# Kernel tuning notes

Measured on AMD Instinct MI355X. Metric: run time of the kernel, lower is better.

Reference implementation:

```python
import jax, jax.numpy as jnp
import numpy as np

D, NH, DH, DHR, DC = 2048, 16, 128, 64, 1024
B, L = 2, 2048
EPS = 1e-6


def _rms(x, w):
    return x * jax.lax.rsqrt(jnp.mean(x * x, axis=-1, keepdims=True) + EPS) * w


def _rope_tables(seq_len, dim, dtype):
    inv_freq = 1.0 / (10000.0 ** (jnp.arange(0, dim, 2, dtype=jnp.float32) / dim))
    freqs = jnp.arange(seq_len, dtype=jnp.float32)[:, None] * inv_freq[None, :]  # [L, dim/2]
    emb = jnp.concatenate([freqs, freqs], axis=-1)                               # [L, dim]
    return jnp.cos(emb).astype(dtype), jnp.sin(emb).astype(dtype)


def _apply_rope(x, cos, sin):
    # x: [B, H, L, dhr]
    half = x.shape[-1] // 2
    x1, x2 = x[..., :half], x[..., half:]
    rot = jnp.concatenate([-x2, x1], axis=-1)
    return x * cos[None, None] + rot * sin[None, None]


def setup_inputs() -> dict:
    key = jax.random.key(0)
    ks = jax.random.split(key, 14)
    s = 0.02
    inp = {
        "x": jax.random.normal(ks[0], (B, L, D), dtype=jnp.float32),
        "W_DKV": jax.random.normal(ks[1], (D, DC), dtype=jnp.float32) * s,
        "kv_norm_w": 1.0 + 0.01 * jax.random.normal(ks[2], (DC,), dtype=jnp.float32),
        "W_UK": jax.random.normal(ks[3], (DC, NH * DH), dtype=jnp.float32) * s,
        "W_UV": jax.random.normal(ks[4], (DC, NH * DH), dtype=jnp.float32) * s,
        "W_DQ": jax.random.normal(ks[5], (D, DC), dtype=jnp.float32) * s,
        "q_norm_w": 1.0 + 0.01 * jax.random.normal(ks[6], (DC,), dtype=jnp.float32),
        "W_UQ": jax.random.normal(ks[7], (DC, 2 * NH * DH), dtype=jnp.float32) * s,
        "W_QR": jax.random.normal(ks[8], (DC, 2 * NH * DHR), dtype=jnp.float32) * s,
        "W_KR": jax.random.normal(ks[9], (D, DHR), dtype=jnp.float32) * s,
        "W_lambda_w": jax.random.normal(ks[10], (D, NH), dtype=jnp.float32) * s,
        "W_lambda_b": jax.random.normal(ks[11], (NH,), dtype=jnp.float32) * s,
        "W_out": jax.random.normal(ks[12], (D, D), dtype=jnp.float32) * s,
    }
    return inp


def reference(x, W_DKV, kv_norm_w, W_UK, W_UV, W_DQ, q_norm_w, W_UQ, W_QR,
              W_KR, W_lambda_w, W_lambda_b, W_out):
    Bx, Lx, Dx = x.shape
    nh, dh, dhr = NH, DH, DHR
    dq = dh + dhr  # per-head query/key dim after decoupled-RoPE concat (192)
    scale = 1.0 / jnp.sqrt(jnp.asarray(dq, dtype=x.dtype))

    # MLA KV path
    c_kv = _rms(x @ W_DKV, kv_norm_w)                                   # [B,L,dc]
    k_c = (c_kv @ W_UK).reshape(Bx, Lx, nh, dh).transpose(0, 2, 1, 3)    # [B,nh,L,dh]
    v = (c_kv @ W_UV).reshape(Bx, Lx, nh, dh).transpose(0, 2, 1, 3)      # [B,nh,L,dh]

    # MLA Q path (doubled heads for Diff V2)
    c_q = _rms(x @ W_DQ, q_norm_w)                                       # [B,L,dcq]
    q_c = (c_q @ W_UQ).reshape(Bx, Lx, 2 * nh, dh).transpose(0, 2, 1, 3)  # [B,2nh,L,dh]

    # Decoupled RoPE
    cos, sin = _rope_tables(Lx, dhr, x.dtype)
    q_r = _apply_rope((c_q @ W_QR).reshape(Bx, Lx, 2 * nh, dhr).transpose(0, 2, 1, 3), cos, sin)
    k_r = _apply_rope((x @ W_KR).reshape(Bx, Lx, 1, dhr).transpose(0, 2, 1, 3), cos, sin)  # [B,1,L,dhr]

    q = jnp.concatenate([q_c, q_r], axis=-1)                             # [B,2nh,L,dq]
    k = jnp.concatenate([k_c, jnp.broadcast_to(k_r, (Bx, nh, Lx, dhr))], axis=-1)  # [B,nh,L,dq]

    # repeat_interleave(2) on K/V == pairing two consecutive Q heads with one K/V head
    qp = q.reshape(Bx, nh, 2, Lx, dq)                                    # [B,nh,2,L,dq]
    scores = jnp.einsum('bnpld,bnmd->bnplm', qp, k) * scale              # [B,nh,2,L,L]
    causal = jnp.tril(jnp.ones((Lx, Lx), dtype=bool))
    scores = jnp.where(causal[None, None, None], scores, jnp.finfo(scores.dtype).min)
    p = jax.nn.softmax(scores, axis=-1)
    attn = jnp.einsum('bnplm,bnmd->bnpld', p, v)                         # [B,nh,2,L,dh]

    attn1, attn2 = attn[:, :, 0], attn[:, :, 1]                          # [B,nh,L,dh]
    lam = jax.nn.sigmoid(x @ W_lambda_w + W_lambda_b)                    # [B,L,nh]
    lam = lam.transpose(0, 2, 1)[..., None]                              # [B,nh,L,1]
    out = (attn1 - lam * attn2).transpose(0, 2, 1, 3).reshape(Bx, Lx, Dx)
    return out @ W_out
```

## Files before the change

kernel.cpp:

```cpp
#include <hip/hip_runtime.h>
#include <cstddef>
#include <cstdint>


namespace {

constexpr int kDC = 1024, kDim = 2048;
constexpr float kScale = 0.07216878364870323f;
constexpr int kTA = 2128;

typedef __bf16 bf16x8 __attribute__((ext_vector_type(8)));
typedef float f32x4 __attribute__((ext_vector_type(4)));

__device__ __forceinline__ unsigned short f2bf(float f) {
  __bf16 h = (__bf16)f;
  return __builtin_bit_cast(unsigned short, h);
}
__device__ __forceinline__ float bf2f(unsigned short h) {
  union { unsigned int u; float f; } v; v.u = ((unsigned int)h) << 16;
  return v.f;
}
__device__ __forceinline__ f32x4 mfma16(bf16x8 a, bf16x8 b, f32x4 c) {
  return __builtin_amdgcn_mfma_f32_16x16x32_bf16(a, b, c, 0, 0, 0);
}
__device__ __forceinline__ void gl_lds16(const void* g, void* l) {
  __builtin_amdgcn_global_load_lds(
      (const __attribute__((address_space(1))) unsigned int*)g,
      (__attribute__((address_space(3))) unsigned int*)l, 16, 0, 0);
}
__device__ __forceinline__ void wait_lgkm0() {
  asm volatile("s_waitcnt lgkmcnt(0)" ::: "memory");
}

__global__ __launch_bounds__(256) void conv_bf16_kernel(const float* __restrict__ in,
                                                        unsigned short* __restrict__ out, int n4) {
  int e = blockIdx.x * 256 + threadIdx.x;
  if (e >= n4) return;
  float4 v = reinterpret_cast<const float4*>(in)[e];
  uint2 pk;
  pk.x = (unsigned int)f2bf(v.x) | ((unsigned int)f2bf(v.y) << 16);
  pk.y = (unsigned int)f2bf(v.z) | ((unsigned int)f2bf(v.w) << 16);
  reinterpret_cast<uint2*>(out)[e] = pk;
}

__global__ __launch_bounds__(256) void zero_bf16_kernel(unsigned short* __restrict__ out, int n8) {
  int e = blockIdx.x * 256 + threadIdx.x;
  if (e >= n8) return;
  reinterpret_cast<uint4*>(out)[e] = uint4{0, 0, 0, 0};
}

__global__ __launch_bounds__(256) void transpose_conv_kernel(const float* __restrict__ in,
                                                             unsigned short* __restrict__ out,
                                                             int K, int N) {
  __shared__ float t[32][33];
  int n0 = blockIdx.x * 32, k0 = blockIdx.y * 32;
  int tx = threadIdx.x & 31, ty = threadIdx.x >> 5;
#pragma unroll
  for (int i = 0; i < 4; i++) t[ty + i * 8][tx] = in[(size_t)(k0 + ty + i * 8) * N + n0 + tx];
  __syncthreads();
#pragma unroll
  for (int i = 0; i < 4; i++)
    out[(size_t)(n0 + ty + i * 8) * K + k0 + tx] = f2bf(t[tx][ty + i * 8]);
}

__global__ __launch_bounds__(256) void lamw_transpose_kernel(const float* __restrict__ in,
                                                             unsigned short* __restrict__ out) {
  int e = blockIdx.x * 256 + threadIdx.x;
  if (e >= 16 * 2048) return;
  int k = e & 2047, n = e >> 11;
  out[(size_t)(2112 + n) * 2048 + k] = f2bf(in[(size_t)k * 16 + n]);
}

template <int MODE>
__device__ __forceinline__ void epi_store(void* dst, void* dst2, int gr, int gc, int N, float v) {
  if (MODE == 0) {
    reinterpret_cast<float*>(dst)[(size_t)gr * N + gc] = v;
  } else if (MODE == 4) {
    if (gc < kTA) reinterpret_cast<float*>(dst)[(size_t)gr * kTA + gc] = v;
  } else if (MODE == 5) {
    int bb = gr >> 11, l = gr & 2047;
    unsigned short hv = f2bf(v);
    if (gc < 2048) {
      int h = gc >> 7, d2 = gc & 127;
      int d2s = d2 ^ ((l & 7) << 3);
      reinterpret_cast<unsigned short*>(dst)[((size_t)((bb * 16 + h) * 2048 + l)) * 192 + d2s] = hv;
    } else {
      int g2 = gc - 2048, h = g2 >> 7, d2 = g2 & 127;
      int ls = l ^ (((d2 >> 1) & 3) << 3);
      reinterpret_cast<unsigned short*>(dst2)[((size_t)((bb * 16 + h) * 128 + d2)) * 2048 + ls] = hv;
    }
  } else if (MODE == 6) {
    int bb = gr >> 11, l = gr & 2047;
    if (gc < 4096) {
      int h2 = gc >> 7, d2 = gc & 127;
      reinterpret_cast<unsigned short*>(dst)[((size_t)((bb * 32 + h2) * 2048 + l)) * 192 + d2] =
          f2bf(v * kScale);
    } else {
      reinterpret_cast<unsigned short*>(dst2)[(size_t)gr * 2048 + (gc - 4096)] = f2bf(v);
    }
  }
}

template <int MODE>
__global__ __launch_bounds__(256) void gemm128_kernel(const unsigned short* __restrict__ A,
                                                      const unsigned short* __restrict__ Bt,
                                                      void* __restrict__ dst, void* __restrict__ dst2,
                                                      int M, int N, int K) {
  __shared__ unsigned short lds_a[128 * 32];
  __shared__ unsigned short lds_b[128 * 32];
  int tid = threadIdx.x, lane = tid & 63, w = tid >> 6;
  int quad = lane >> 4, l16 = lane & 15;
  int wr = w >> 1, wc = w & 1;
  int nwg = gridDim.x * gridDim.y;
  int bid = blockIdx.y * gridDim.x + blockIdx.x;
  int cpx = nwg >> 3;
  int swz = (bid & 7) * cpx + (bid >> 3);
  int bx = swz % gridDim.x, by = swz / gridDim.x;
  int mbase = by * 128, nbase = bx * 128;
  f32x4 acc[4][4] = {};
  int srow0 = tid >> 2, skoff = (tid & 3) * 8;
  const size_t a_base = (size_t)(mbase + srow0) * K + skoff;
  const size_t b_base = (size_t)(nbase + srow0) * K + skoff;
  unsigned short* lba0 = &lds_a[(size_t)(w * 64) * 8];
  unsigned short* lba1 = &lds_a[(size_t)(256 + w * 64) * 8];
  unsigned short* lbb0 = &lds_b[(size_t)(w * 64) * 8];
  unsigned short* lbb1 = &lds_b[(size_t)(256 + w * 64) * 8];
  for (int k0 = 0; k0 < K; k0 += 32) {
    __syncthreads();
    gl_lds16(&A[a_base + k0], lba0);
    gl_lds16(&A[a_base + (size_t)64 * K + k0], lba1);
    gl_lds16(&Bt[b_base + k0], lbb0);
    gl_lds16(&Bt[b_base + (size_t)64 * K + k0], lbb1);
    __syncthreads();
    bf16x8 af[4], bfr[4];
#pragma unroll
    for (int i = 0; i < 4; i++) {
      af[i] = *reinterpret_cast<const bf16x8*>(&lds_a[(wr * 64 + i * 16 + l16) * 32 + quad * 8]);
      bfr[i] = *reinterpret_cast<const bf16x8*>(&lds_b[(wc * 64 + i * 16 + l16) * 32 + quad * 8]);
    }
#pragma unroll
    for (int i = 0; i < 4; i++)
#pragma unroll
      for (int j = 0; j < 4; j++) acc[i][j] = mfma16(af[i], bfr[j], acc[i][j]);
  }
#pragma unroll
  for (int i = 0; i < 4; i++)
#pragma unroll
    for (int j = 0; j < 4; j++)
#pragma unroll
      for (int r = 0; r < 4; r++) {
        int gr = mbase + wr * 64 + i * 16 + quad * 4 + r;
        int gc = nbase + wc * 64 + j * 16 + l16;
        epi_store<MODE>(dst, dst2, gr, gc, N, acc[i][j][r]);
      }
}

__global__ __launch_bounds__(256) void rms_kernel(const float* __restrict__ in,
                                                  const float* __restrict__ w,
                                                  unsigned short* __restrict__ out, int colOff) {
  int row = blockIdx.x, tid = threadIdx.x;
  float4 v = reinterpret_cast<const float4*>(in + (size_t)row * kTA + colOff)[tid];
  float ss = v.x * v.x + v.y * v.y + v.z * v.z + v.w * v.w;
  ss += __shfl_xor(ss, 1); ss += __shfl_xor(ss, 2); ss += __shfl_xor(ss, 4);
  ss += __shfl_xor(ss, 8); ss += __shfl_xor(ss, 16); ss += __shfl_xor(ss, 32);
  __shared__ float red[4];
  if ((tid & 63) == 0) red[tid >> 6] = ss;
  __syncthreads();
  float tot = red[0] + red[1] + red[2] + red[3];
  float rs = rsqrtf(tot * (1.0f / kDC) + 1e-6f);
  float4 wv = reinterpret_cast<const float4*>(w)[tid];
  uint2 pk;
  pk.x = (unsigned int)f2bf(v.x * rs * wv.x) | ((unsigned int)f2bf(v.y * rs * wv.y) << 16);
  pk.y = (unsigned int)f2bf(v.z * rs * wv.z) | ((unsigned int)f2bf(v.w * rs * wv.w) << 16);
  reinterpret_cast<uint2*>(out)[(size_t)row * 256 + tid] = pk;
}

__device__ __forceinline__ float rope_val(float x1, float x2, int j, int l) {
  int i = j & 31;
  float inv_freq = powf(10000.0f, -(float)i * (1.0f / 32.0f));
  float ang = (float)l * inv_freq;
  float cv = cosf(ang), sv = sinf(ang);
  float rot = (j < 32) ? -x2 : x2;
  return x1 * cv + rot * sv;
}

__global__ __launch_bounds__(256) void rope_q_kernel(const unsigned short* __restrict__ qr_raw,
                                                     unsigned short* __restrict__ q_all) {
  size_t e = (size_t)blockIdx.x * 256 + threadIdx.x;
  int j = (int)(e & 63);
  int h2 = (int)((e >> 6) & 31);
  int bl = (int)(e >> 11);
  int l = bl & 2047, b = bl >> 11;
  float x1 = bf2f(qr_raw[(size_t)bl * 2048 + h2 * 64 + j]);
  float x2 = bf2f(qr_raw[(size_t)bl * 2048 + h2 * 64 + (j ^ 32)]);
  float val = rope_val(x1, x2, j, l) * kScale;
  q_all[((size_t)((b * 32 + h2) * 2048 + l)) * 192 + 128 + j] = f2bf(val);
}

__global__ __launch_bounds__(256) void rope_k_kernel(const float* __restrict__ tmpAll,
                                                     unsigned short* __restrict__ k_all) {
  size_t e = (size_t)blockIdx.x * 256 + threadIdx.x;
  int j = (int)(e & 63);
  int bl = (int)(e >> 6);
  int l = bl & 2047, b = bl >> 11;
  float x1 = tmpAll[(size_t)bl * kTA + 2048 + j];
  float x2 = tmpAll[(size_t)bl * kTA + 2048 + (j ^ 32)];
  unsigned short hv = f2bf(rope_val(x1, x2, j, l));
  int js = j ^ ((l & 7) << 3);
#pragma unroll
  for (int h = 0; h < 16; h++)
    k_all[((size_t)((b * 16 + h) * 2048 + l)) * 192 + 128 + js] = hv;
}

__global__ __launch_bounds__(256) void lam_fin_kernel(const float* __restrict__ tmpAll,
                                                      const float* __restrict__ bl_,
                                                      float* __restrict__ lam) {
  int e = blockIdx.x * 256 + threadIdx.x;
  if (e >= 4096 * 16) return;
  int n = e & 15, row = e >> 4;
  float z = tmpAll[(size_t)row * kTA + 2112 + n] + bl_[n];
  lam[e] = 1.f / (1.f + __expf(-z));
}

__global__ __launch_bounds__(256, 3) void attn3_kernel(const unsigned short* __restrict__ q_all,
                                                       const unsigned short* __restrict__ k_all,
                                                       const unsigned short* __restrict__ v_allT,
                                                       unsigned short* __restrict__ attn_o) {
  __shared__ unsigned short lds_k[2][32 * 192];
  __shared__ unsigned short lds_v[2][128 * 32];
  __shared__ unsigned short lds_p[8 * 640];
  __shared__ unsigned short lds_ones[16 * 32];
  int n = blockIdx.x, qp = blockIdx.y, b = blockIdx.z;
  int tid = threadIdx.x, lane = tid & 63, w = tid >> 6, quad = lane >> 4, l16 = lane & 15;
  const unsigned short* k_head = k_all + ((size_t)(b * 16 + n) * 2048) * 192;
  const unsigned short* v_head = v_allT + ((size_t)(b * 16 + n) * 128) * 2048;

  for (int idx = tid; idx < 512; idx += 256)
    lds_ones[idx] = (idx < 32) ? (unsigned short)0x3F80 : (unsigned short)0;

  unsigned short* pw0 = &lds_p[(w * 2 + 0) * 640];
  unsigned short* pw1 = &lds_p[(w * 2 + 1) * 640];

  auto stage = [&](int pos0, int buf) {
    const unsigned short* kg = k_head + (size_t)pos0 * 192 + w * 1536 + lane * 8;
    unsigned short* kl = &lds_k[buf][w * 1536];
    gl_lds16(kg, kl);
    gl_lds16(kg + 512, kl + 512);
    gl_lds16(kg + 1024, kl + 1024);
    const unsigned short* vg =
        v_head + (size_t)(w * 32 + (lane >> 2)) * 2048 + pos0 + (lane & 3) * 8;
    unsigned short* vl = &lds_v[buf][w * 1024];
    gl_lds16(vg, vl);
    gl_lds16(vg + (size_t)16 * 2048, vl + 512);
  };

#pragma unroll 1
  for (int phase = 0; phase < 2; ++phase) {
    int qt = phase ? qp : (31 - qp);
    const unsigned short* q0_row =
        q_all + ((size_t)(b * 32 + 2 * n) * 2048 + qt * 64 + w * 16 + l16) * 192;
    const unsigned short* q1_row = q0_row + (size_t)2048 * 192;

    bf16x8 qf0[6], qf1[6];
#pragma unroll
    for (int ks = 0; ks < 6; ks++) {
      qf0[ks] = *reinterpret_cast<const bf16x8*>(&q0_row[ks * 32 + quad * 8]);
      qf1[ks] = *reinterpret_cast<const bf16x8*>(&q1_row[ks * 32 + quad * 8]);
    }

    f32x4 acc0[9] = {}, acc1[9] = {};
    int qlo = qt * 64 + w * 16;
    int nt = 2 * qt + 2;

    stage(0, 0);
    for (int kt = 0; kt < nt; kt++) {
      int cur = kt & 1;
      int pos0 = kt * 32;
      __syncthreads();
      if (kt + 1 < nt) stage((kt + 1) * 32, cur ^ 1);
      if (pos0 <= qlo + 15) {
        const unsigned short* kb = &lds_k[cur][0];
        const unsigned short* vb = &lds_v[cur][0];
        bool needmask = (pos0 + 31 > qlo);
        int ksw = (l16 & 7) << 3;
        int vsw = (l16 >> 1) & 3;
#pragma unroll
        for (int j = 0; j < 2; j++) {
          f32x4 s0 = {}, s1 = {};
#pragma unroll
          for (int ks = 0; ks < 6; ks++) {
            bf16x8 bK = *reinterpret_cast<const bf16x8*>(
                &kb[(j * 16 + l16) * 192 + ((ks * 32 + quad * 8) ^ ksw)]);
            s0 = mfma16(qf0[ks], bK, s0);
            s1 = mfma16(qf1[ks], bK, s1);
          }
#pragma unroll
          for (int r = 0; r < 4; r++) {
            bool msk = needmask && (pos0 + j * 16 + l16 > qlo + quad * 4 + r);
            float p0 = msk ? 0.f : __expf(s0[r]);
            float p1 = msk ? 0.f : __expf(s1[r]);
            pw0[(quad * 4 + r) * 40 + j * 16 + l16] = f2bf(p0);
            pw1[(quad * 4 + r) * 40 + j * 16 + l16] = f2bf(p1);
          }
        }
        wait_lgkm0();
        bf16x8 pf0 = *reinterpret_cast<const bf16x8*>(&pw0[l16 * 40 + quad * 8]);
        bf16x8 pf1 = *reinterpret_cast<const bf16x8*>(&pw1[l16 * 40 + quad * 8]);
#pragma unroll
        for (int dt = 0; dt < 8; dt++) {
          bf16x8 vf = *reinterpret_cast<const bf16x8*>(
              &vb[(dt * 16 + l16) * 32 + ((quad ^ vsw) * 8)]);
          acc0[dt] = mfma16(pf0, vf, acc0[dt]);
          acc1[dt] = mfma16(pf1, vf, acc1[dt]);
        }
        bf16x8 vone = *reinterpret_cast<const bf16x8*>(&lds_ones[l16 * 32 + quad * 8]);
        acc0[8] = mfma16(pf0, vone, acc0[8]);
        acc1[8] = mfma16(pf1, vone, acc1[8]);
      }
    }

    unsigned short* o0 = attn_o + ((size_t)(b * 32 + 2 * n) * 2048 + qt * 64 + w * 16) * 128;
    unsigned short* o1 = o0 + (size_t)2048 * 128;
#pragma unroll
    for (int r = 0; r < 4; r++) {
      float li0 = __shfl(acc0[8][r], lane & 48);
      float li1 = __shfl(acc1[8][r], lane & 48);
      float inv0 = 1.f / li0, inv1 = 1.f / li1;
      int row = quad * 4 + r;
#pragma unroll
      for (int dt = 0; dt < 8; dt++) {
        o0[(size_t)row * 128 + dt * 16 + l16] = f2bf(acc0[dt][r] * inv0);
        o1[(size_t)row * 128 + dt * 16 + l16] = f2bf(acc1[dt][r] * inv1);
      }
    }
  }
}

__global__ __launch_bounds__(256) void combine_kernel(const unsigned short* __restrict__ attn_o,
                                                      const float* __restrict__ lam,
                                                      unsigned short* __restrict__ out) {
  size_t e = (size_t)blockIdx.x * 256 + threadIdx.x;
  int c8 = (int)(e & 255);
  int bl = (int)(e >> 8);
  int n = c8 >> 4, dd = (c8 & 15) * 8;
  int b = bl >> 11, l = bl & 2047;
  size_t base = ((size_t)((b * 32 + n * 2) * 2048 + l)) * 128 + dd;
  uint4 a1 = *reinterpret_cast<const uint4*>(attn_o + base);
  uint4 a2 = *reinterpret_cast<const uint4*>(attn_o + base + (size_t)2048 * 128);
  float lm = lam[(size_t)bl * 16 + n];
  unsigned int r[4];
  const unsigned int* p1 = &a1.x;
  const unsigned int* p2 = &a2.x;
#pragma unroll
  for (int i = 0; i < 4; i++) {
    float lo = bf2f((unsigned short)(p1[i] & 0xFFFF)) - lm * bf2f((unsigned short)(p2[i] & 0xFFFF));
    float hi = bf2f((unsigned short)(p1[i] >> 16)) - lm * bf2f((unsigned short)(p2[i] >> 16));
    r[i] = (unsigned int)f2bf(lo) | ((unsigned int)f2bf(hi) << 16);
  }
  *reinterpret_cast<uint4*>(out + e * 8) = uint4{r[0], r[1], r[2], r[3]};
}

}

extern "C" void kernel_launch(void* const* d_in, const int* in_sizes, int n_in,
                              void* d_out, int out_size, void* d_ws, size_t ws_size,
                              hipStream_t stream) {
  const float* x      = (const float*)d_in[0];
  const float* W_DKV  = (const float*)d_in[1];
  const float* kvnw   = (const float*)d_in[2];
  const float* W_UK   = (const float*)d_in[3];
  const float* W_UV   = (const float*)d_in[4];
  const float* W_DQ   = (const float*)d_in[5];
  const float* qnw    = (const float*)d_in[6];
  const float* W_UQ   = (const float*)d_in[7];
  const float* W_QR   = (const float*)d_in[8];
  const float* W_KR   = (const float*)d_in[9];
  const float* W_lw   = (const float*)d_in[10];
  const float* W_lb   = (const float*)d_in[11];
  const float* W_out  = (const float*)d_in[12];
  float* out = (float*)d_out;

  char* ws = (char*)d_ws;
  size_t off = 0;
  auto alloc = [&](size_t bytes) { char* p = ws + off; off += (bytes + 255) & ~(size_t)255; return p; };
  unsigned short* xb     = (unsigned short*)alloc((size_t)4096 * 2048 * 2);
  unsigned short* wd_cat = (unsigned short*)alloc((size_t)2176 * 2048 * 2);
  unsigned short* wu_cat = (unsigned short*)alloc((size_t)4096 * 1024 * 2);
  unsigned short* wuqr   = (unsigned short*)alloc((size_t)6144 * 1024 * 2);
  unsigned short* wout   = (unsigned short*)alloc((size_t)2048 * 2048 * 2);
  unsigned short* ckv    = (unsigned short*)alloc((size_t)4096 * 1024 * 2);
  unsigned short* cq     = (unsigned short*)alloc((size_t)4096 * 1024 * 2);
  unsigned short* k_all  = (unsigned short*)alloc((size_t)2 * 16 * 2048 * 192 * 2);
  unsigned short* v_allT = (unsigned short*)alloc((size_t)2 * 16 * 128 * 2048 * 2);
  unsigned short* q_all  = (unsigned short*)alloc((size_t)2 * 32 * 2048 * 192 * 2);
  unsigned short* attn_o = (unsigned short*)alloc((size_t)2 * 32 * 2048 * 128 * 2);
  unsigned short* attn_b = (unsigned short*)alloc((size_t)4096 * 2048 * 2);
  float* lam             = (float*)alloc((size_t)4096 * 16 * 4);
  float* tmpAll          = (float*)alloc((size_t)4096 * kTA * 4);
  unsigned short* tmpB   = (unsigned short*)tmpAll;
  (void)ws_size; (void)in_sizes; (void)n_in; (void)out_size;

  hipLaunchKernelGGL(conv_bf16_kernel, dim3(8192), dim3(256), 0, stream, x, xb, 2097152);
  hipLaunchKernelGGL(transpose_conv_kernel, dim3(32, 64), dim3(256), 0, stream, W_DKV, wd_cat, 2048, 1024);
  hipLaunchKernelGGL(transpose_conv_kernel, dim3(32, 64), dim3(256), 0, stream, W_DQ,
                     wd_cat + (size_t)1024 * 2048, 2048, 1024);
  hipLaunchKernelGGL(transpose_conv_kernel, dim3(2, 64), dim3(256), 0, stream, W_KR,
                     wd_cat + (size_t)2048 * 2048, 2048, 64);
  hipLaunchKernelGGL(lamw_transpose_kernel, dim3(128), dim3(256), 0, stream, W_lw, wd_cat);
  hipLaunchKernelGGL(zero_bf16_kernel, dim3(48), dim3(256), 0, stream,
                     wd_cat + (size_t)2128 * 2048, 12288);
  hipLaunchKernelGGL(transpose_conv_kernel, dim3(64, 32), dim3(256), 0, stream, W_UK, wu_cat, 1024, 2048);
  hipLaunchKernelGGL(transpose_conv_kernel, dim3(64, 32), dim3(256), 0, stream, W_UV,
                     wu_cat + (size_t)2048 * 1024, 1024, 2048);
  hipLaunchKernelGGL(transpose_conv_kernel, dim3(128, 32), dim3(256), 0, stream, W_UQ, wuqr, 1024, 4096);
  hipLaunchKernelGGL(transpose_conv_kernel, dim3(64, 32), dim3(256), 0, stream, W_QR,
                     wuqr + (size_t)4096 * 1024, 1024, 2048);
  hipLaunchKernelGGL(transpose_conv_kernel, dim3(64, 64), dim3(256), 0, stream, W_out, wout, 2048, 2048);

  hipLaunchKernelGGL(gemm128_kernel<4>, dim3(17, 32), dim3(256), 0, stream,
                     xb, wd_cat, tmpAll, (void*)nullptr, 4096, 2176, 2048);
  hipLaunchKernelGGL(rms_kernel, dim3(4096), dim3(256), 0, stream, tmpAll, kvnw, ckv, 0);
  hipLaunchKernelGGL(rms_kernel, dim3(4096), dim3(256), 0, stream, tmpAll, qnw, cq, 1024);
  hipLaunchKernelGGL(rope_k_kernel, dim3(1024), dim3(256), 0, stream, tmpAll, k_all);
  hipLaunchKernelGGL(lam_fin_kernel, dim3(256), dim3(256), 0, stream, tmpAll, W_lb, lam);

  hipLaunchKernelGGL(gemm128_kernel<5>, dim3(32, 32), dim3(256), 0, stream,
                     ckv, wu_cat, k_all, v_allT, 4096, 4096, 1024);
  hipLaunchKernelGGL(gemm128_kernel<6>, dim3(48, 32), dim3(256), 0, stream,
                     cq, wuqr, q_all, tmpB, 4096, 6144, 1024);
  hipLaunchKernelGGL(rope_q_kernel, dim3(32768), dim3(256), 0, stream, tmpB, q_all);

  hipLaunchKernelGGL(attn3_kernel, dim3(16, 16, 2), dim3(256), 0, stream,
                     q_all, k_all, v_allT, attn_o);

  hipLaunchKernelGGL(combine_kernel, dim3(4096), dim3(256), 0, stream, attn_o, lam, attn_b);
  hipLaunchKernelGGL(gemm128_kernel<0>, dim3(16, 32), dim3(256), 0, stream,
                     attn_b, wout, out, (void*)nullptr, 4096, 2048, 2048);
}
```

Before: 666.6 us.

## Load V fragments directly from global memory instead of staging through LDS

```diff
diff --git a/kernel.cpp b/kernel.cpp
--- a/kernel.cpp
+++ b/kernel.cpp
@@ -86,8 +86,7 @@
       reinterpret_cast<unsigned short*>(dst)[((size_t)((bb * 16 + h) * 2048 + l)) * 192 + d2s] = hv;
     } else {
       int g2 = gc - 2048, h = g2 >> 7, d2 = g2 & 127;
-      int ls = l ^ (((d2 >> 1) & 3) << 3);
-      reinterpret_cast<unsigned short*>(dst2)[((size_t)((bb * 16 + h) * 128 + d2)) * 2048 + ls] = hv;
+      reinterpret_cast<unsigned short*>(dst2)[((size_t)((bb * 16 + h) * 128 + d2)) * 2048 + l] = hv;
     }
   } else if (MODE == 6) {
     int bb = gr >> 11, l = gr & 2047;
@@ -222,36 +221,30 @@
   lam[e] = 1.f / (1.f + __expf(-z));
 }
 
-__global__ __launch_bounds__(256, 3) void attn3_kernel(const unsigned short* __restrict__ q_all,
+__global__ __launch_bounds__(256, 2) void attn7_kernel(const unsigned short* __restrict__ q_all,
                                                        const unsigned short* __restrict__ k_all,
                                                        const unsigned short* __restrict__ v_allT,
                                                        unsigned short* __restrict__ attn_o) {
   __shared__ unsigned short lds_k[2][32 * 192];
-  __shared__ unsigned short lds_v[2][128 * 32];
   __shared__ unsigned short lds_p[8 * 640];
-  __shared__ unsigned short lds_ones[16 * 32];
   int n = blockIdx.x, qp = blockIdx.y, b = blockIdx.z;
   int tid = threadIdx.x, lane = tid & 63, w = tid >> 6, quad = lane >> 4, l16 = lane & 15;
   const unsigned short* k_head = k_all + ((size_t)(b * 16 + n) * 2048) * 192;
   const unsigned short* v_head = v_allT + ((size_t)(b * 16 + n) * 128) * 2048;
 
-  for (int idx = tid; idx < 512; idx += 256)
-    lds_ones[idx] = (idx < 32) ? (unsigned short)0x3F80 : (unsigned short)0;
-
   unsigned short* pw0 = &lds_p[(w * 2 + 0) * 640];
   unsigned short* pw1 = &lds_p[(w * 2 + 1) * 640];
-
-  auto stage = [&](int pos0, int buf) {
+  const unsigned short* v_lane = v_head + (size_t)l16 * 2048 + quad * 8;
+
+  __bf16 onec = __builtin_bit_cast(__bf16, (unsigned short)(l16 == 0 ? 0x3F80 : 0));
+  bf16x8 vone = {onec, onec, onec, onec, onec, onec, onec, onec};
+
+  auto stageK = [&](int pos0, int buf) {
     const unsigned short* kg = k_head + (size_t)pos0 * 192 + w * 1536 + lane * 8;
     unsigned short* kl = &lds_k[buf][w * 1536];
     gl_lds16(kg, kl);
     gl_lds16(kg + 512, kl + 512);
     gl_lds16(kg + 1024, kl + 1024);
-    const unsigned short* vg =
-        v_head + (size_t)(w * 32 + (lane >> 2)) * 2048 + pos0 + (lane & 3) * 8;
-    unsigned short* vl = &lds_v[buf][w * 1024];
-    gl_lds16(vg, vl);
-    gl_lds16(vg + (size_t)16 * 2048, vl + 512);
   };
 
 #pragma unroll 1
@@ -272,18 +265,25 @@
     int qlo = qt * 64 + w * 16;
     int nt = 2 * qt + 2;
 
-    stage(0, 0);
+    stageK(0, 0);
     for (int kt = 0; kt < nt; kt++) {
       int cur = kt & 1;
       int pos0 = kt * 32;
       __syncthreads();
-      if (kt + 1 < nt) stage((kt + 1) * 32, cur ^ 1);
-      if (pos0 <= qlo + 15) {
+      bool active = (pos0 <= qlo + 15);
+      bf16x8 vf[8];
+      if (active) {
+        const unsigned short* vg = v_lane + pos0;
+#pragma unroll
+        for (int dt = 0; dt < 8; dt++)
+          vf[dt] = *reinterpret_cast<const bf16x8*>(&vg[(size_t)dt * 16 * 2048]);
+      }
+      __builtin_amdgcn_sched_barrier(0);
+      if (kt + 1 < nt) stageK((kt + 1) * 32, cur ^ 1);
+      if (active) {
         const unsigned short* kb = &lds_k[cur][0];
-        const unsigned short* vb = &lds_v[cur][0];
         bool needmask = (pos0 + 31 > qlo);
         int ksw = (l16 & 7) << 3;
-        int vsw = (l16 >> 1) & 3;
 #pragma unroll
         for (int j = 0; j < 2; j++) {
           f32x4 s0 = {}, s1 = {};
@@ -308,12 +308,9 @@
         bf16x8 pf1 = *reinterpret_cast<const bf16x8*>(&pw1[l16 * 40 + quad * 8]);
 #pragma unroll
         for (int dt = 0; dt < 8; dt++) {
-          bf16x8 vf = *reinterpret_cast<const bf16x8*>(
-              &vb[(dt * 16 + l16) * 32 + ((quad ^ vsw) * 8)]);
-          acc0[dt] = mfma16(pf0, vf, acc0[dt]);
-          acc1[dt] = mfma16(pf1, vf, acc1[dt]);
+          acc0[dt] = mfma16(pf0, vf[dt], acc0[dt]);
+          acc1[dt] = mfma16(pf1, vf[dt], acc1[dt]);
         }
-        bf16x8 vone = *reinterpret_cast<const bf16x8*>(&lds_ones[l16 * 32 + quad * 8]);
         acc0[8] = mfma16(pf0, vone, acc0[8]);
         acc1[8] = mfma16(pf1, vone, acc1[8]);
       }
@@ -430,7 +427,7 @@
                      cq, wuqr, q_all, tmpB, 4096, 6144, 1024);
   hipLaunchKernelGGL(rope_q_kernel, dim3(32768), dim3(256), 0, stream, tmpB, q_all);
 
-  hipLaunchKernelGGL(attn3_kernel, dim3(16, 16, 2), dim3(256), 0, stream,
+  hipLaunchKernelGGL(attn7_kernel, dim3(16, 16, 2), dim3(256), 0, stream,
                      q_all, k_all, v_allT, attn_o);
 
   hipLaunchKernelGGL(combine_kernel, dim3(4096), dim3(256), 0, stream, attn_o, lam, attn_b);
```

After: 676.9 us. No clear change (+1.5%).
